# Kernel tuning notes

Hardware: AMD Instinct MI355X
Metric: run time of the kernel (lower is better)

The kernel has to match this reference:

```python
import jax, jax.numpy as jnp
import numpy as np

T, EMB, OUT = 4096, 2048, 2048


def setup_inputs() -> dict:
    key = jax.random.key(0)
    ks = jax.random.split(key, 7)
    s = 1.0 / np.sqrt(OUT)  # PyTorch LSTMCell init scale (values only; math identical)
    return {
        "stacked_info": jax.random.normal(ks[0], (T, EMB), jnp.float32),
        "init_hid": jax.random.normal(ks[1], (OUT,), jnp.float32),
        "init_cell": jax.random.normal(ks[2], (OUT,), jnp.float32),
        "W_ih": jax.random.uniform(ks[3], (4 * OUT, EMB), jnp.float32, -s, s),
        "W_hh": jax.random.uniform(ks[4], (4 * OUT, OUT), jnp.float32, -s, s),
        "b_ih": jax.random.uniform(ks[5], (4 * OUT,), jnp.float32, -s, s),
        "b_hh": jax.random.uniform(ks[6], (4 * OUT,), jnp.float32, -s, s),
    }


def reference(stacked_info, init_hid, init_cell, W_ih, W_hh, b_ih, b_hh):
    # Precompute input projections for all timesteps in one GEMM: [T, 4*OUT]
    x_proj = stacked_info @ W_ih.T + b_ih + b_hh

    def step(carry, xp):
        h, c = carry  # each [OUT]
        gates = xp + h @ W_hh.T  # [4*OUT]; PyTorch gate order: i, f, g, o
        i, f, g, o = jnp.split(gates, 4)
        i = jax.nn.sigmoid(i)
        f = jax.nn.sigmoid(f)
        g = jnp.tanh(g)
        o = jax.nn.sigmoid(o)
        c = f * c + i * g
        h = o * jnp.tanh(c)
        return (h, c), None

    (h, c), _ = jax.lax.scan(step, (init_hid, init_cell), x_proj)
    return (h, c)
```

## Files before the change

kernel.cpp:

```cpp
#include <hip/hip_runtime.h>
#include <hip/hip_bf16.h>

typedef __attribute__((ext_vector_type(8))) short short8;
typedef __attribute__((ext_vector_type(4))) float f32x4;

#define T_STEPS 4096
#define EMBD 2048
#define OUTD 2048
#define N4 8192
#define NBLK 256
#define WPB 8

#define AL(p) __hip_atomic_load((p), __ATOMIC_RELAXED, __HIP_MEMORY_SCOPE_AGENT)

__device__ __forceinline__ unsigned int pack_h(float h, unsigned int tag) {
    unsigned int u = __float_as_uint(h);
    u += 0x7fffu + ((u >> 16) & 1u);
    return (u & 0xffff0000u) | (tag & 0xffffu);
}

__global__ void f32_to_bf16_kernel(const float* __restrict__ in,
                                   __hip_bfloat16* __restrict__ out, int n) {
    int i = blockIdx.x * blockDim.x + threadIdx.x;
    int stride = gridDim.x * blockDim.x;
    for (int idx = i * 4; idx < n; idx += stride * 4) {
        float4 v = *(const float4*)(in + idx);
        out[idx + 0] = __float2bfloat16(v.x);
        out[idx + 1] = __float2bfloat16(v.y);
        out[idx + 2] = __float2bfloat16(v.z);
        out[idx + 3] = __float2bfloat16(v.w);
    }
}

__global__ void prep_kernel(const float* __restrict__ init_hid,
                            unsigned int* __restrict__ hbuf2) {
    int i = blockIdx.x * blockDim.x + threadIdx.x;
    if (i < OUTD) {
        hbuf2[i] = pack_h(init_hid[i], 0u);
        hbuf2[OUTD + i] = 0u;
    }
}

__global__ __launch_bounds__(256) void gemm_xproj(
    const __hip_bfloat16* __restrict__ A, const __hip_bfloat16* __restrict__ B,
    const float* __restrict__ b_ih, const float* __restrict__ b_hh,
    __hip_bfloat16* __restrict__ xp) {
    __shared__ __hip_bfloat16 As[64][32];
    __shared__ __hip_bfloat16 Bs[64][32];
    const int bm = blockIdx.x, bn = blockIdx.y;
    const int tid = threadIdx.x;
    const int w = tid >> 6, l = tid & 63;
    const int wr = w >> 1, wc = w & 1;
    const int srow = tid >> 2, skc = tid & 3;

    f32x4 acc[2][2] = {};

    const __hip_bfloat16* Abase = A + (size_t)(bm * 64 + srow) * EMBD + skc * 8;
    const __hip_bfloat16* Bbase = B + (size_t)(bn * 64 + srow) * EMBD + skc * 8;

    const int krow = l >> 4;
    const int fr = l & 15;

    for (int k0 = 0; k0 < EMBD; k0 += 32) {
        __syncthreads();
        *(short8*)(&As[srow][skc * 8]) = *(const short8*)(Abase + k0);
        *(short8*)(&Bs[srow][skc * 8]) = *(const short8*)(Bbase + k0);
        __syncthreads();

        short8 afrag[2], bfrag[2];
#pragma unroll
        for (int m = 0; m < 2; ++m)
            afrag[m] = *(const short8*)(&As[wr * 32 + m * 16 + fr][krow * 8]);
#pragma unroll
        for (int n = 0; n < 2; ++n)
            bfrag[n] = *(const short8*)(&Bs[wc * 32 + n * 16 + fr][krow * 8]);
#pragma unroll
        for (int m = 0; m < 2; ++m)
#pragma unroll
            for (int n = 0; n < 2; ++n)
                acc[m][n] = __builtin_amdgcn_mfma_f32_16x16x32_bf16(
                    afrag[m], bfrag[n], acc[m][n], 0, 0, 0);
    }

    const int fq = l >> 4;
#pragma unroll
    for (int m = 0; m < 2; ++m) {
#pragma unroll
        for (int n = 0; n < 2; ++n) {
            int col = bn * 64 + wc * 32 + n * 16 + fr;
            float bias = b_ih[col] + b_hh[col];
#pragma unroll
            for (int r = 0; r < 4; ++r) {
                int row = bm * 64 + wr * 32 + m * 16 + fq * 4 + r;
                xp[(size_t)row * N4 + col] = __float2bfloat16(acc[m][n][r] + bias);
            }
        }
    }
}

__global__ __launch_bounds__(512, 2) void lstm_scan(
    const float* __restrict__ W_hh,
    const __hip_bfloat16* __restrict__ xp,
    const float* __restrict__ init_cell,
    unsigned int* hbuf2,
    float* __restrict__ out)
{
    __shared__ float hs[2][OUTD];
    const int tid = threadIdx.x;
    const int wave = tid >> 6;
    const int lane = tid & 63;
    const int j = blockIdx.x * WPB + wave;
    const int chunk = wave * 256 + lane;

    float Wreg[4][32];
#pragma unroll
    for (int rr = 0; rr < 4; ++rr) {
        const float* wrow = W_hh + (size_t)(rr * OUTD + j) * OUTD;
#pragma unroll
        for (int kk = 0; kk < 32; ++kk)
            Wreg[rr][kk] = wrow[kk * 64 + lane];
    }
    float c = init_cell[j];

    for (int t = 0; t < T_STEPS; ++t) {
        const unsigned int tag = (unsigned int)t;
        const int pr = t & 1;
        unsigned int* hsrc = hbuf2 + (size_t)pr * OUTD;

        const __hip_bfloat16* xpt = xp + (size_t)t * N4 + j;
        float xpi = __bfloat162float(xpt[0]);
        float xpf = __bfloat162float(xpt[OUTD]);
        float xpg = __bfloat162float(xpt[2 * OUTD]);
        float xpo = __bfloat162float(xpt[3 * OUTD]);

        unsigned int w0, w1, w2, w3;
        {
            int spins = 0;
            bool rmw = false;
            while (true) {
                if (!rmw) {
                    w0 = AL(&hsrc[chunk]);
                    w1 = AL(&hsrc[chunk + 64]);
                    w2 = AL(&hsrc[chunk + 128]);
                    w3 = AL(&hsrc[chunk + 192]);
                } else {
                    w0 = __hip_atomic_fetch_add(&hsrc[chunk],       0u, __ATOMIC_RELAXED, __HIP_MEMORY_SCOPE_AGENT);
                    w1 = __hip_atomic_fetch_add(&hsrc[chunk + 64],  0u, __ATOMIC_RELAXED, __HIP_MEMORY_SCOPE_AGENT);
                    w2 = __hip_atomic_fetch_add(&hsrc[chunk + 128], 0u, __ATOMIC_RELAXED, __HIP_MEMORY_SCOPE_AGENT);
                    w3 = __hip_atomic_fetch_add(&hsrc[chunk + 192], 0u, __ATOMIC_RELAXED, __HIP_MEMORY_SCOPE_AGENT);
                }
                bool ok = ((w0 & 0xffffu) == tag) & ((w1 & 0xffffu) == tag) &
                          ((w2 & 0xffffu) == tag) & ((w3 & 0xffffu) == tag);
                if (__all(ok)) break;
                if (++spins > 8) __builtin_amdgcn_s_sleep(1);
                if (spins > 100000) rmw = true;
            }
        }
        hs[pr][chunk]       = __uint_as_float(w0 & 0xffff0000u);
        hs[pr][chunk + 64]  = __uint_as_float(w1 & 0xffff0000u);
        hs[pr][chunk + 128] = __uint_as_float(w2 & 0xffff0000u);
        hs[pr][chunk + 192] = __uint_as_float(w3 & 0xffff0000u);
        __syncthreads();

        float acc0 = 0.f, acc1 = 0.f, acc2 = 0.f, acc3 = 0.f;
#pragma unroll
        for (int kk = 0; kk < 32; ++kk) {
            float hval = hs[pr][kk * 64 + lane];
            acc0 += Wreg[0][kk] * hval;
            acc1 += Wreg[1][kk] * hval;
            acc2 += Wreg[2][kk] * hval;
            acc3 += Wreg[3][kk] * hval;
        }
#pragma unroll
        for (int s = 32; s >= 1; s >>= 1) {
            acc0 += __shfl_xor(acc0, s);
            acc1 += __shfl_xor(acc1, s);
            acc2 += __shfl_xor(acc2, s);
            acc3 += __shfl_xor(acc3, s);
        }

        float gi = __builtin_amdgcn_rcpf(1.f + __expf(-(xpi + acc0)));
        float gf = __builtin_amdgcn_rcpf(1.f + __expf(-(xpf + acc1)));
        float gg = 1.f - 2.f * __builtin_amdgcn_rcpf(__expf(2.f * (xpg + acc2)) + 1.f);
        float go = __builtin_amdgcn_rcpf(1.f + __expf(-(xpo + acc3)));
        c = gf * c + gi * gg;
        float h = go * (1.f - 2.f * __builtin_amdgcn_rcpf(__expf(2.f * c) + 1.f));

        if (t == T_STEPS - 1) {
            if (lane == 0) { out[j] = h; out[OUTD + j] = c; }
        } else if (lane == 0) {
            unsigned int packed = pack_h(h, (unsigned int)(t + 1));
            (void)__hip_atomic_exchange(&hbuf2[(size_t)((t + 1) & 1) * OUTD + j],
                                        packed, __ATOMIC_RELAXED,
                                        __HIP_MEMORY_SCOPE_AGENT);
        }
    }
}

extern "C" void kernel_launch(void* const* d_in, const int* in_sizes, int n_in,
                              void* d_out, int out_size, void* d_ws, size_t ws_size,
                              hipStream_t stream) {
    (void)in_sizes; (void)n_in; (void)out_size; (void)ws_size;
    const float* stacked   = (const float*)d_in[0];
    const float* init_hid  = (const float*)d_in[1];
    const float* init_cell = (const float*)d_in[2];
    const float* W_ih      = (const float*)d_in[3];
    const float* W_hh      = (const float*)d_in[4];
    const float* b_ih      = (const float*)d_in[5];
    const float* b_hh      = (const float*)d_in[6];
    float* out = (float*)d_out;

    char* ws = (char*)d_ws;
    __hip_bfloat16* xp  = (__hip_bfloat16*)ws;
    __hip_bfloat16* A16 = (__hip_bfloat16*)(ws + 67108864);
    __hip_bfloat16* W16 = (__hip_bfloat16*)(ws + 83886080);
    unsigned int* hbuf2 = (unsigned int*)(ws + 117440512);

    f32_to_bf16_kernel<<<4096, 256, 0, stream>>>(stacked, A16, T_STEPS * EMBD);
    f32_to_bf16_kernel<<<8192, 256, 0, stream>>>(W_ih, W16, N4 * EMBD);
    prep_kernel<<<8, 256, 0, stream>>>(init_hid, hbuf2);
    gemm_xproj<<<dim3(64, 128), 256, 0, stream>>>(A16, W16, b_ih, b_hh, xp);
    lstm_scan<<<NBLK, 512, 0, stream>>>(W_hh, xp, init_cell, hbuf2, out);
}
```

Baseline: 7.991 ms.

## Relay hidden state through per-XCC staging buffer elected per chiplet

Measured after the change: 15.63 ms. +95.6%, slower.

```diff
diff --git a/kernel.cpp b/kernel.cpp
--- a/kernel.cpp
+++ b/kernel.cpp
@@ -12,6 +12,9 @@
 #define WPB 8
 
 #define AL(p) __hip_atomic_load((p), __ATOMIC_RELAXED, __HIP_MEMORY_SCOPE_AGENT)
+#define ARMW(p) __hip_atomic_fetch_add((p), 0u, __ATOMIC_RELAXED, __HIP_MEMORY_SCOPE_AGENT)
+#define AST(p, v) __hip_atomic_store((p), (v), __ATOMIC_RELAXED, __HIP_MEMORY_SCOPE_AGENT)
+#define VLD(p) (*(volatile const unsigned int*)(p))
 
 __device__ __forceinline__ unsigned int pack_h(float h, unsigned int tag) {
     unsigned int u = __float_as_uint(h);
@@ -33,12 +36,21 @@
 }
 
 __global__ void prep_kernel(const float* __restrict__ init_hid,
-                            unsigned int* __restrict__ hbuf2) {
+                            unsigned int* __restrict__ hbuf2,
+                            unsigned int* __restrict__ stage,
+                            int* __restrict__ slots) {
     int i = blockIdx.x * blockDim.x + threadIdx.x;
     if (i < OUTD) {
-        hbuf2[i] = pack_h(init_hid[i], 0u);
+        unsigned int p0 = pack_h(init_hid[i], 0u);
+        hbuf2[i] = p0;
         hbuf2[OUTD + i] = 0u;
-    }
+#pragma unroll
+        for (int x = 0; x < 8; ++x) {
+            stage[(size_t)(x * 2 + 0) * OUTD + i] = p0;
+            stage[(size_t)(x * 2 + 1) * OUTD + i] = 0u;
+        }
+    }
+    if (i < 8) slots[i] = 0;
 }
 
 __global__ __launch_bounds__(256) void gemm_xproj(
@@ -103,15 +115,23 @@
     const __hip_bfloat16* __restrict__ xp,
     const float* __restrict__ init_cell,
     unsigned int* hbuf2,
+    unsigned int* stage,
+    int* slots,
     float* __restrict__ out)
 {
     __shared__ float hs[2][OUTD];
+    __shared__ int relayFlagLds;
     const int tid = threadIdx.x;
     const int wave = tid >> 6;
     const int lane = tid & 63;
     const int j = blockIdx.x * WPB + wave;
     const int chunk = wave * 256 + lane;
 
+    int xcc;
+    asm volatile("s_getreg_b32 %0, hwreg(HW_REG_XCC_ID)" : "=s"(xcc));
+    xcc &= 7;
+    if (tid == 0) relayFlagLds = (atomicCAS(&slots[xcc], 0, 1) == 0) ? 1 : 0;
+
     float Wreg[4][32];
 #pragma unroll
     for (int rr = 0; rr < 4; ++rr) {
@@ -121,11 +141,15 @@
             Wreg[rr][kk] = wrow[kk * 64 + lane];
     }
     float c = init_cell[j];
+    __syncthreads();
+    const bool isRelay = (relayFlagLds != 0);
+    bool useGlobal = false;
 
     for (int t = 0; t < T_STEPS; ++t) {
         const unsigned int tag = (unsigned int)t;
         const int pr = t & 1;
         unsigned int* hsrc = hbuf2 + (size_t)pr * OUTD;
+        unsigned int* sbase = stage + (((size_t)xcc * 2 + pr) << 11);
 
         const __hip_bfloat16* xpt = xp + (size_t)t * N4 + j;
         float xpi = __bfloat162float(xpt[0]);
@@ -134,26 +158,43 @@
         float xpo = __bfloat162float(xpt[3 * OUTD]);
 
         unsigned int w0, w1, w2, w3;
-        {
-            int spins = 0;
-            bool rmw = false;
+        if (isRelay) {
+            int spins = 0; bool rmw = false;
             while (true) {
                 if (!rmw) {
-                    w0 = AL(&hsrc[chunk]);
-                    w1 = AL(&hsrc[chunk + 64]);
-                    w2 = AL(&hsrc[chunk + 128]);
-                    w3 = AL(&hsrc[chunk + 192]);
+                    w0 = AL(&hsrc[chunk]);       w1 = AL(&hsrc[chunk + 64]);
+                    w2 = AL(&hsrc[chunk + 128]); w3 = AL(&hsrc[chunk + 192]);
                 } else {
-                    w0 = __hip_atomic_fetch_add(&hsrc[chunk],       0u, __ATOMIC_RELAXED, __HIP_MEMORY_SCOPE_AGENT);
-                    w1 = __hip_atomic_fetch_add(&hsrc[chunk + 64],  0u, __ATOMIC_RELAXED, __HIP_MEMORY_SCOPE_AGENT);
-                    w2 = __hip_atomic_fetch_add(&hsrc[chunk + 128], 0u, __ATOMIC_RELAXED, __HIP_MEMORY_SCOPE_AGENT);
-                    w3 = __hip_atomic_fetch_add(&hsrc[chunk + 192], 0u, __ATOMIC_RELAXED, __HIP_MEMORY_SCOPE_AGENT);
+                    w0 = ARMW(&hsrc[chunk]);       w1 = ARMW(&hsrc[chunk + 64]);
+                    w2 = ARMW(&hsrc[chunk + 128]); w3 = ARMW(&hsrc[chunk + 192]);
                 }
                 bool ok = ((w0 & 0xffffu) == tag) & ((w1 & 0xffffu) == tag) &
                           ((w2 & 0xffffu) == tag) & ((w3 & 0xffffu) == tag);
                 if (__all(ok)) break;
                 if (++spins > 8) __builtin_amdgcn_s_sleep(1);
                 if (spins > 100000) rmw = true;
+            }
+            AST(&sbase[chunk], w0);       AST(&sbase[chunk + 64], w1);
+            AST(&sbase[chunk + 128], w2); AST(&sbase[chunk + 192], w3);
+        } else {
+            int spins = 0; bool rmw = false;
+            while (true) {
+                if (!useGlobal) {
+                    w0 = VLD(&sbase[chunk]);       w1 = VLD(&sbase[chunk + 64]);
+                    w2 = VLD(&sbase[chunk + 128]); w3 = VLD(&sbase[chunk + 192]);
+                } else if (!rmw) {
+                    w0 = AL(&hsrc[chunk]);       w1 = AL(&hsrc[chunk + 64]);
+                    w2 = AL(&hsrc[chunk + 128]); w3 = AL(&hsrc[chunk + 192]);
+                } else {
+                    w0 = ARMW(&hsrc[chunk]);       w1 = ARMW(&hsrc[chunk + 64]);
+                    w2 = ARMW(&hsrc[chunk + 128]); w3 = ARMW(&hsrc[chunk + 192]);
+                }
+                bool ok = ((w0 & 0xffffu) == tag) & ((w1 & 0xffffu) == tag) &
+                          ((w2 & 0xffffu) == tag) & ((w3 & 0xffffu) == tag);
+                if (__all(ok)) break;
+                if (++spins > 8) __builtin_amdgcn_s_sleep(1);
+                if (!useGlobal && spins > 256) { useGlobal = true; spins = 9; }
+                if (useGlobal && spins > 100000) rmw = true;
             }
         }
         hs[pr][chunk]       = __uint_as_float(w0 & 0xffff0000u);
@@ -215,10 +256,12 @@
     __hip_bfloat16* A16 = (__hip_bfloat16*)(ws + 67108864);
     __hip_bfloat16* W16 = (__hip_bfloat16*)(ws + 83886080);
     unsigned int* hbuf2 = (unsigned int*)(ws + 117440512);
+    unsigned int* stage = (unsigned int*)(ws + 117456896);
+    int* slots          = (int*)(ws + 117587968);
 
     f32_to_bf16_kernel<<<4096, 256, 0, stream>>>(stacked, A16, T_STEPS * EMBD);
     f32_to_bf16_kernel<<<8192, 256, 0, stream>>>(W_ih, W16, N4 * EMBD);
-    prep_kernel<<<8, 256, 0, stream>>>(init_hid, hbuf2);
+    prep_kernel<<<8, 256, 0, stream>>>(init_hid, hbuf2, stage, slots);
     gemm_xproj<<<dim3(64, 128), 256, 0, stream>>>(A16, W16, b_ih, b_hh, xp);
-    lstm_scan<<<NBLK, 512, 0, stream>>>(W_hh, xp, init_cell, hbuf2, out);
-}
+    lstm_scan<<<NBLK, 512, 0, stream>>>(W_hh, xp, init_cell, hbuf2, stage, slots, out);
+}
```
